# Performance work log

Measured on AMD Instinct MI355X. Metric: run time of the kernel, lower is better.

The kernel has to match this reference:

```python
import jax, jax.numpy as jnp
import numpy as np

N, K = 8192, 64          # num pixels (b*h*w), proj_dim
C, M = 19, 10            # num_classes, num_prototype


def setup_inputs() -> dict:
    key = jax.random.key(0)
    k1, k2, k3 = jax.random.split(key, 3)
    x = jax.random.normal(k1, (N, K), dtype=jnp.float32)
    x_var = jax.random.uniform(k2, (N, K), dtype=jnp.float32)  # positive variances
    proto_mean = jax.random.normal(k3, (C, M, K), dtype=jnp.float32) * 0.02  # trunc_normal std=0.02
    proto_var = jnp.ones((C, M, K), dtype=jnp.float32)
    return {"x": x, "x_var": x_var, "proto_mean": proto_mean, "proto_var": proto_var}


def reference(x, x_var, proto_mean, proto_var):
    # MLS similarity: sim = -0.5 * mean_k[ (mu - x)^2 / (sig_x + sig_p) + log(sig_x + sig_p) ]
    pm = proto_mean[:, :, None, :]            # (c, m, 1, k)
    pv = proto_var[:, :, None, :]             # (c, m, 1, k)
    mean_diff = jnp.square(pm - x)            # (c, m, n, k) broadcast
    var_sum = x_var + pv                      # (c, m, n, k)
    sim = mean_diff / var_sum + jnp.log(var_sum)
    sim = -0.5 * jnp.mean(sim, axis=-1)       # (c, m, n)
    return jnp.transpose(sim, (2, 0, 1))      # (n, c, m) == permute(2, 0, 1)
```

## Files before the change

kernel.cpp:

```cpp
#include <hip/hip_runtime.h>

#define NROWS 8192
#define KDIM 64
#define CDIM 19
#define MDIM 10
#define CMDIM (CDIM * MDIM)
#define CM_PER_BLOCK 19
#define ROWS_PER_BLOCK 64
#define LDS_STRIDE 65

__global__ __launch_bounds__(256)
void probproto_kernel(const float* __restrict__ x,
                      const float* __restrict__ xv,
                      const float* __restrict__ pm,
                      const float* __restrict__ pv,
                      float* __restrict__ out)
{
    __shared__ float xs_t[KDIM * LDS_STRIDE];
    __shared__ float xvs_t[KDIM * LDS_STRIDE];
    __shared__ float pms[CM_PER_BLOCK * KDIM];
    __shared__ float pvs[CM_PER_BLOCK * KDIM];

    const int t   = threadIdx.x;
    const int n0  = blockIdx.x * ROWS_PER_BLOCK;
    const int cm0 = blockIdx.y * CM_PER_BLOCK;

    const float4* x4  = (const float4*)(x  + (size_t)n0 * KDIM);
    const float4* xv4 = (const float4*)(xv + (size_t)n0 * KDIM);
    #pragma unroll
    for (int i = 0; i < 4; ++i) {
        int idx = t + 256 * i;
        int r   = idx >> 4;
        int c4  = idx & 15;
        float4 a = x4[idx];
        float4 b = xv4[idx];
        int k = c4 * 4;
        xs_t[(k + 0) * LDS_STRIDE + r] = a.x;
        xs_t[(k + 1) * LDS_STRIDE + r] = a.y;
        xs_t[(k + 2) * LDS_STRIDE + r] = a.z;
        xs_t[(k + 3) * LDS_STRIDE + r] = a.w;
        xvs_t[(k + 0) * LDS_STRIDE + r] = b.x;
        xvs_t[(k + 1) * LDS_STRIDE + r] = b.y;
        xvs_t[(k + 2) * LDS_STRIDE + r] = b.z;
        xvs_t[(k + 3) * LDS_STRIDE + r] = b.w;
    }
    for (int idx = t; idx < CM_PER_BLOCK * KDIM; idx += 256) {
        pms[idx] = pm[cm0 * KDIM + idx];
        pvs[idx] = pv[cm0 * KDIM + idx];
    }
    __syncthreads();

    const int wave = t >> 6;
    const int lane = t & 63;
    const int n    = n0 + lane;

    for (int cmi = wave; cmi < CM_PER_BLOCK; cmi += 4) {
        float accQ = 0.0f;
        float accL = 0.0f;
        for (int kc = 0; kc < 4; ++kc) {
            float prod = 1.0f;
            #pragma unroll
            for (int k8 = 0; k8 < 16; ++k8) {
                int k = kc * 16 + k8;
                float pmv = pms[cmi * KDIM + k];
                float pvv = pvs[cmi * KDIM + k];
                float xx  = xs_t[k * LDS_STRIDE + lane];
                float xvv = xvs_t[k * LDS_STRIDE + lane];
                float v = xvv + pvv;
                float d = pmv - xx;
                accQ = fmaf(d * d, __builtin_amdgcn_rcpf(v), accQ);
                prod *= v;
            }
            accL += __log2f(prod);
        }
        out[(size_t)n * CMDIM + cm0 + cmi] =
            -(accQ + 0.69314718055994531f * accL) * (1.0f / 128.0f);
    }
}

extern "C" void kernel_launch(void* const* d_in, const int* in_sizes, int n_in,
                              void* d_out, int out_size, void* d_ws, size_t ws_size,
                              hipStream_t stream) {
    const float* x  = (const float*)d_in[0];
    const float* xv = (const float*)d_in[1];
    const float* pm = (const float*)d_in[2];
    const float* pv = (const float*)d_in[3];
    float* out = (float*)d_out;

    dim3 grid(NROWS / ROWS_PER_BLOCK, CMDIM / CM_PER_BLOCK);
    probproto_kernel<<<grid, 256, 0, stream>>>(x, xv, pm, pv, out);
}
```

Before: 84.45 us.

## Keep each pixel's x and variance in registers, read prototypes via scalar loads

The shared-memory staging of transposed x/x_var and prototype tiles is removed. Each 64-thread block now loads one pixel row per lane into 128 registers and walks 10 prototypes, whose values are wave-uniform and so can become scalar loads. The grid becomes 19 class tiles by 128 row tiles, and accumulation is split into 4 independent chains to expose ILP. In exchange, register pressure is high, x is re-read by 19 blocks, and the per-lane row loads and output writes are strided and uncoalesced.

```diff
diff --git a/kernel.cpp b/kernel.cpp
--- a/kernel.cpp
+++ b/kernel.cpp
@@ -1,80 +1,55 @@
 #include <hip/hip_runtime.h>
 
 #define NROWS 8192
-#define KDIM 64
-#define CDIM 19
-#define MDIM 10
-#define CMDIM (CDIM * MDIM)
-#define CM_PER_BLOCK 19
-#define ROWS_PER_BLOCK 64
-#define LDS_STRIDE 65
+#define KDIM  64
+#define CMDIM 190
+#define CMT   10
+#define NCT   19
 
-__global__ __launch_bounds__(256)
+__global__ __launch_bounds__(64)
 void probproto_kernel(const float* __restrict__ x,
                       const float* __restrict__ xv,
                       const float* __restrict__ pm,
                       const float* __restrict__ pv,
                       float* __restrict__ out)
 {
-    __shared__ float xs_t[KDIM * LDS_STRIDE];
-    __shared__ float xvs_t[KDIM * LDS_STRIDE];
-    __shared__ float pms[CM_PER_BLOCK * KDIM];
-    __shared__ float pvs[CM_PER_BLOCK * KDIM];
+    const int lane = threadIdx.x;
+    const int ct   = blockIdx.x;
+    const int n    = blockIdx.y * 64 + lane;
 
-    const int t   = threadIdx.x;
-    const int n0  = blockIdx.x * ROWS_PER_BLOCK;
-    const int cm0 = blockIdx.y * CM_PER_BLOCK;
+    float xr[KDIM], vr[KDIM];
+    const float4* xp = (const float4*)(x  + (size_t)n * KDIM);
+    const float4* vp = (const float4*)(xv + (size_t)n * KDIM);
+    #pragma unroll
+    for (int i = 0; i < KDIM / 4; ++i) {
+        float4 a = xp[i], b = vp[i];
+        xr[4*i+0] = a.x; xr[4*i+1] = a.y; xr[4*i+2] = a.z; xr[4*i+3] = a.w;
+        vr[4*i+0] = b.x; vr[4*i+1] = b.y; vr[4*i+2] = b.z; vr[4*i+3] = b.w;
+    }
 
-    const float4* x4  = (const float4*)(x  + (size_t)n0 * KDIM);
-    const float4* xv4 = (const float4*)(xv + (size_t)n0 * KDIM);
-    #pragma unroll
-    for (int i = 0; i < 4; ++i) {
-        int idx = t + 256 * i;
-        int r   = idx >> 4;
-        int c4  = idx & 15;
-        float4 a = x4[idx];
-        float4 b = xv4[idx];
-        int k = c4 * 4;
-        xs_t[(k + 0) * LDS_STRIDE + r] = a.x;
-        xs_t[(k + 1) * LDS_STRIDE + r] = a.y;
-        xs_t[(k + 2) * LDS_STRIDE + r] = a.z;
-        xs_t[(k + 3) * LDS_STRIDE + r] = a.w;
-        xvs_t[(k + 0) * LDS_STRIDE + r] = b.x;
-        xvs_t[(k + 1) * LDS_STRIDE + r] = b.y;
-        xvs_t[(k + 2) * LDS_STRIDE + r] = b.z;
-        xvs_t[(k + 3) * LDS_STRIDE + r] = b.w;
-    }
-    for (int idx = t; idx < CM_PER_BLOCK * KDIM; idx += 256) {
-        pms[idx] = pm[cm0 * KDIM + idx];
-        pvs[idx] = pv[cm0 * KDIM + idx];
-    }
-    __syncthreads();
+    float* orow = out + (size_t)n * CMDIM + ct * CMT;
 
-    const int wave = t >> 6;
-    const int lane = t & 63;
-    const int n    = n0 + lane;
+    for (int j = 0; j < CMT; ++j) {
+        const float* pmr = pm + (size_t)(ct * CMT + j) * KDIM;
+        const float* pvr = pv + (size_t)(ct * CMT + j) * KDIM;
 
-    for (int cmi = wave; cmi < CM_PER_BLOCK; cmi += 4) {
-        float accQ = 0.0f;
-        float accL = 0.0f;
+        float q[4] = {0.f, 0.f, 0.f, 0.f};
+        float accL = 0.f;
+        #pragma unroll
         for (int kc = 0; kc < 4; ++kc) {
-            float prod = 1.0f;
+            float p[4] = {1.f, 1.f, 1.f, 1.f};
             #pragma unroll
             for (int k8 = 0; k8 < 16; ++k8) {
                 int k = kc * 16 + k8;
-                float pmv = pms[cmi * KDIM + k];
-                float pvv = pvs[cmi * KDIM + k];
-                float xx  = xs_t[k * LDS_STRIDE + lane];
-                float xvv = xvs_t[k * LDS_STRIDE + lane];
-                float v = xvv + pvv;
-                float d = pmv - xx;
-                accQ = fmaf(d * d, __builtin_amdgcn_rcpf(v), accQ);
-                prod *= v;
+                float v = vr[k] + pvr[k];
+                float d = pmr[k] - xr[k];
+                q[k8 & 3] = fmaf(d * d, __builtin_amdgcn_rcpf(v), q[k8 & 3]);
+                p[k8 & 3] *= v;
             }
-            accL += __log2f(prod);
+            accL += __log2f((p[0] * p[1]) * (p[2] * p[3]));
         }
-        out[(size_t)n * CMDIM + cm0 + cmi] =
-            -(accQ + 0.69314718055994531f * accL) * (1.0f / 128.0f);
+        orow[j] = -(((q[0] + q[1]) + (q[2] + q[3]))
+                    + 0.69314718055994531f * accL) * (1.0f / 128.0f);
     }
 }
 
@@ -87,6 +62,6 @@
     const float* pv = (const float*)d_in[3];
     float* out = (float*)d_out;
 
-    dim3 grid(NROWS / ROWS_PER_BLOCK, CMDIM / CM_PER_BLOCK);
-    probproto_kernel<<<grid, 256, 0, stream>>>(x, xv, pm, pv, out);
+    dim3 grid(NCT, NROWS / 64);
+    probproto_kernel<<<grid, 64, 0, stream>>>(x, xv, pm, pv, out);
 }
```

Result: slower. 92.43 us (+9.4%).
